# Optimization experiments

Measured on AMD Instinct MI355X. Metric: run time of the kernel, lower is better.

Reference implementation:

```python
import jax, jax.numpy as jnp
import numpy as np

EMBED_DIM = 2048
NUM_HEADS = 32
HEAD_DIM = EMBED_DIM // NUM_HEADS  # 64; only used as softmax scale
BATCH = 2
SEQ_LEN = 2048


def setup_inputs() -> dict:
    key = jax.random.key(0)
    ks = jax.random.split(key, 5)
    scale = 1.0 / np.sqrt(EMBED_DIM)
    x = jax.random.normal(ks[0], (BATCH, SEQ_LEN, EMBED_DIM), dtype=jnp.float32)
    Wq = jax.random.normal(ks[1], (EMBED_DIM, EMBED_DIM), dtype=jnp.float32) * scale
    Wk = jax.random.normal(ks[2], (EMBED_DIM, EMBED_DIM), dtype=jnp.float32) * scale
    Wv = jax.random.normal(ks[3], (EMBED_DIM, EMBED_DIM), dtype=jnp.float32) * scale
    Wo = jax.random.normal(ks[4], (EMBED_DIM, EMBED_DIM), dtype=jnp.float32) * scale
    return {"x": x, "Wq": Wq, "Wk": Wk, "Wv": Wv, "Wo": Wo}


def reference(x, Wq, Wk, Wv, Wo):
    # x: [b, s, e]
    q = jnp.einsum('bse,ef->bsf', x, Wq)  # [b, s, e]
    k = jnp.einsum('bse,ef->bsf', x, Wk)
    v = jnp.einsum('bse,ef->bsf', x, Wv)
    # NOTE: original transposes (1,2) WITHOUT splitting heads, so "attention"
    # is over the embed dimension: q^T k -> [b, e, e]
    qT = jnp.swapaxes(q, 1, 2)  # [b, e, s]
    kT = jnp.swapaxes(k, 1, 2)  # [b, e, s]
    vT = jnp.swapaxes(v, 1, 2)  # [b, e, s]
    attn_scores = jnp.einsum('bes,bfs->bef', qT, kT) / np.sqrt(HEAD_DIM)  # [b,e,e]
    attn_weights = jax.nn.softmax(attn_scores, axis=-1)
    attn_output = jnp.einsum('bef,bfs->bes', attn_weights, vT)  # [b, e, s]
    attn_output = jnp.swapaxes(attn_output, 1, 2)  # [b, s, e]
    return jnp.einsum('bse,ef->bsf', attn_output, Wo)
```

## Files before the change

kernel.cpp:

```cpp
#include <hip/hip_runtime.h>
#include <cstddef>
#include <cstdint>

constexpr int E     = 2048;
constexpr int SEQ   = 2048;
constexpr int BATCH = 2;
constexpr int BS    = BATCH * SEQ;

constexpr int BM = 128, BN = 128, BK = 64;

typedef _Float16 f16;
typedef f16  f16x4 __attribute__((ext_vector_type(4)));
typedef f16  f16x8 __attribute__((ext_vector_type(8)));
typedef float f32x4 __attribute__((ext_vector_type(4)));

#define GLOAD16(g, l)                                                   \
    __builtin_amdgcn_global_load_lds(                                   \
        (const __attribute__((address_space(1))) void*)(g),             \
        (__attribute__((address_space(3))) void*)(l), 16, 0, 0)

template <int EPI, typename CT>
__global__ __launch_bounds__(256) void gemm_f16(
    const f16* __restrict__ A, const f16* __restrict__ B, CT* __restrict__ C,
    int K, int lda, int ldb, int ldc,
    long long sA, long long sB, long long sC, float alpha)
{
    alignas(16) __shared__ f16 At[BM * BK];
    alignas(16) __shared__ f16 Bt[BN * BK];

    const int tid = threadIdx.x;
    const int l   = tid & 63;
    const int w   = tid >> 6;

    const int nwg  = gridDim.x * gridDim.y;
    const int flat = blockIdx.y * gridDim.x + blockIdx.x;
    const int cpx  = nwg >> 3;
    const int swz  = (flat & 7) * cpx + (flat >> 3);
    const int bx = swz % gridDim.x, by = swz / gridDim.x;
    const int m0 = by * BM, n0 = bx * BN;

    const f16* Ab = A + (size_t)blockIdx.z * sA;
    const f16* Bb = B + (size_t)blockIdx.z * sB;

    const int lr = l & 15;
    const int hi = l >> 4;
    const int wm = (w >> 1) * 64;
    const int wn = (w & 1) * 64;

    f32x4 acc[4][4] = {};

    for (int k0 = 0; k0 < K; k0 += BK) {
#pragma unroll
        for (int p = 0; p < 4; ++p) {
            const int ci  = p * 256 + tid;
            const int row = ci >> 3;
            const int sc  = (ci & 7) ^ (row & 7);
            GLOAD16(Ab + (size_t)(m0 + row) * lda + k0 + sc * 8,
                    At + p * 2048 + w * 512);
            GLOAD16(Bb + (size_t)(n0 + row) * ldb + k0 + sc * 8,
                    Bt + p * 2048 + w * 512);
        }
        __syncthreads();

        f16x8 af[4][2], bf[4][2];
#pragma unroll
        for (int i = 0; i < 4; ++i)
#pragma unroll
            for (int ks = 0; ks < 2; ++ks) {
                const int ar = wm + i * 16 + lr;
                const int ap = (ks * 4 + hi) ^ (ar & 7);
                af[i][ks] = *reinterpret_cast<const f16x8*>(At + ar * 64 + ap * 8);
                const int br = wn + i * 16 + lr;
                const int bp = (ks * 4 + hi) ^ (br & 7);
                bf[i][ks] = *reinterpret_cast<const f16x8*>(Bt + br * 64 + bp * 8);
            }
#pragma unroll
        for (int ks = 0; ks < 2; ++ks)
#pragma unroll
            for (int i = 0; i < 4; ++i)
#pragma unroll
                for (int j = 0; j < 4; ++j)
                    acc[i][j] = __builtin_amdgcn_mfma_f32_16x16x32_f16(
                        af[i][ks], bf[j][ks], acc[i][j], 0, 0, 0);
        __syncthreads();
    }

    if (EPI == 0) {
        CT* Cb = C + (size_t)blockIdx.z * sC;
#pragma unroll
        for (int i = 0; i < 4; ++i)
#pragma unroll
            for (int r = 0; r < 4; ++r) {
                const int row = m0 + wm + i * 16 + hi * 4 + r;
#pragma unroll
                for (int j = 0; j < 4; ++j) {
                    const int col = n0 + wn + j * 16 + lr;
                    Cb[(size_t)row * ldc + col] = (CT)(alpha * acc[i][j][r]);
                }
            }
    } else {
        f16* Cb = (f16*)C;
#pragma unroll
        for (int i = 0; i < 4; ++i) {
            const int rowb = m0 + wm + i * 16 + hi * 4;
            const long long base = ((long long)(rowb >> 11) << 22) + (rowb & 2047);
#pragma unroll
            for (int j = 0; j < 4; ++j) {
                const int col = n0 + wn + j * 16 + lr;
                f16x4 v = {(f16)(alpha * acc[i][j][0]), (f16)(alpha * acc[i][j][1]),
                           (f16)(alpha * acc[i][j][2]), (f16)(alpha * acc[i][j][3])};
                *reinterpret_cast<f16x4*>(Cb + base + (long long)col * 2048) = v;
            }
        }
    }
}

__global__ __launch_bounds__(256) void conv_x_f16(
    const float* __restrict__ x, f16* __restrict__ xc, int n4)
{
    int i = blockIdx.x * 256 + threadIdx.x;
    const int stride = gridDim.x * 256;
    for (; i < n4; i += stride) {
        const float4 v = reinterpret_cast<const float4*>(x)[i];
        f16x4 h = {(f16)v.x, (f16)v.y, (f16)v.z, (f16)v.w};
        reinterpret_cast<f16x4*>(xc)[i] = h;
    }
}

__global__ __launch_bounds__(256) void conv_wT(
    const float* __restrict__ W0, const float* __restrict__ W1,
    const float* __restrict__ W2, const float* __restrict__ W3,
    f16* __restrict__ O0, f16* __restrict__ O1,
    f16* __restrict__ O2, f16* __restrict__ O3)
{
    const float* src; f16* dst;
    switch (blockIdx.z) {
        case 0: src = W0; dst = O0; break;
        case 1: src = W1; dst = O1; break;
        case 2: src = W2; dst = O2; break;
        default: src = W3; dst = O3; break;
    }
    __shared__ f16 t[64][68];
    const int e0 = blockIdx.y * 64, f0 = blockIdx.x * 64;
    const int tid = threadIdx.x;
    const int tf = (tid & 15) * 4;
    const int te = tid >> 4;
#pragma unroll
    for (int p = 0; p < 4; ++p) {
        const int e = te + p * 16;
        const float4 v = *reinterpret_cast<const float4*>(
            &src[(size_t)(e0 + e) * 2048 + f0 + tf]);
        t[tf + 0][e] = (f16)v.x; t[tf + 1][e] = (f16)v.y;
        t[tf + 2][e] = (f16)v.z; t[tf + 3][e] = (f16)v.w;
    }
    __syncthreads();
#pragma unroll
    for (int p = 0; p < 4; ++p) {
        const int f = (tid >> 4) + p * 16;
        const int e = (tid & 15) * 4;
        const f16x4 v = *reinterpret_cast<const f16x4*>(&t[f][e]);
        *reinterpret_cast<f16x4*>(&dst[(size_t)(f0 + f) * 2048 + e0 + e]) = v;
    }
}

__global__ __launch_bounds__(256) void softmax_rows_f16(
    const float* __restrict__ S, f16* __restrict__ A)
{
    const float* row = S + (size_t)blockIdx.x * 2048;
    f16* arow = A + (size_t)blockIdx.x * 2048;
    const int tid = threadIdx.x;

    float4 v0 = reinterpret_cast<const float4*>(row)[tid];
    float4 v1 = reinterpret_cast<const float4*>(row)[tid + 256];

    float m = fmaxf(fmaxf(fmaxf(v0.x, v0.y), fmaxf(v0.z, v0.w)),
                    fmaxf(fmaxf(v1.x, v1.y), fmaxf(v1.z, v1.w)));
#pragma unroll
    for (int off = 32; off > 0; off >>= 1) m = fmaxf(m, __shfl_xor(m, off));

    __shared__ float red[8];
    if ((tid & 63) == 0) red[tid >> 6] = m;
    __syncthreads();
    m = fmaxf(fmaxf(red[0], red[1]), fmaxf(red[2], red[3]));

    v0.x = __expf(v0.x - m); v0.y = __expf(v0.y - m);
    v0.z = __expf(v0.z - m); v0.w = __expf(v0.w - m);
    v1.x = __expf(v1.x - m); v1.y = __expf(v1.y - m);
    v1.z = __expf(v1.z - m); v1.w = __expf(v1.w - m);

    float s = v0.x + v0.y + v0.z + v0.w + v1.x + v1.y + v1.z + v1.w;
#pragma unroll
    for (int off = 32; off > 0; off >>= 1) s += __shfl_xor(s, off);
    if ((tid & 63) == 0) red[4 + (tid >> 6)] = s;
    __syncthreads();
    s = red[4] + red[5] + red[6] + red[7];

    const float inv = 1.0f / s;
    f16x4 a0 = {(f16)(v0.x * inv), (f16)(v0.y * inv), (f16)(v0.z * inv), (f16)(v0.w * inv)};
    f16x4 a1 = {(f16)(v1.x * inv), (f16)(v1.y * inv), (f16)(v1.z * inv), (f16)(v1.w * inv)};
    reinterpret_cast<f16x4*>(arow)[tid]       = a0;
    reinterpret_cast<f16x4*>(arow)[tid + 256] = a1;
}

extern "C" void kernel_launch(void* const* d_in, const int* in_sizes, int n_in,
                              void* d_out, int out_size, void* d_ws, size_t ws_size,
                              hipStream_t stream)
{
    const float* x  = (const float*)d_in[0];
    const float* Wq = (const float*)d_in[1];
    const float* Wk = (const float*)d_in[2];
    const float* Wv = (const float*)d_in[3];
    const float* Wo = (const float*)d_in[4];
    float* out = (float*)d_out;

    f16* ws16 = (f16*)d_ws;
    const size_t MATE = (size_t)BS * E;
    const size_t WMAT = (size_t)E * E;
    f16* xc  = ws16;
    f16* WqT = xc  + MATE;
    f16* WkT = WqT + WMAT;
    f16* WvT = WkT + WMAT;
    f16* WoT = WvT + WMAT;
    f16* QT  = WoT + WMAT;
    f16* KT  = QT  + MATE;
    f16* V   = KT  + MATE;
    float* S = (float*)(V + MATE);
    f16* A   = QT;
    f16* AO  = KT;

    const dim3 blk(256);
    const long long BMATL = (long long)E * E;

    hipLaunchKernelGGL(conv_x_f16, dim3(2048), blk, 0, stream, x, xc, (int)(MATE / 4));
    hipLaunchKernelGGL(conv_wT, dim3(32, 32, 4), blk, 0, stream,
                       Wq, Wk, Wv, Wo, WqT, WkT, WvT, WoT);

    const dim3 gBig(E / BN, BS / BM, 1);
    const dim3 gSq (E / BN, E  / BM, BATCH);

    hipLaunchKernelGGL((gemm_f16<1, f16>), gBig, blk, 0, stream,
                       xc, WqT, QT, E, E, E, E, 0LL, 0LL, 0LL, 1.0f);
    hipLaunchKernelGGL((gemm_f16<1, f16>), gBig, blk, 0, stream,
                       xc, WkT, KT, E, E, E, E, 0LL, 0LL, 0LL, 1.0f);
    hipLaunchKernelGGL((gemm_f16<0, f16>), gBig, blk, 0, stream,
                       xc, WvT, V, E, E, E, E, 0LL, 0LL, 0LL, 1.0f);

    hipLaunchKernelGGL((gemm_f16<0, float>), gSq, blk, 0, stream,
                       QT, KT, S, SEQ, E, E, E, BMATL, BMATL, BMATL, 0.125f);

    hipLaunchKernelGGL(softmax_rows_f16, dim3(BATCH * E), blk, 0, stream, S, A);

    hipLaunchKernelGGL((gemm_f16<0, f16>), gSq, blk, 0, stream,
                       V, A, AO, E, E, E, E, BMATL, BMATL, BMATL, 1.0f);

    hipLaunchKernelGGL((gemm_f16<0, float>), gBig, blk, 0, stream,
                       AO, WoT, out, E, E, E, E, 0LL, 0LL, 0LL, 1.0f);
}
```

Before: 412.3 us.

## Double-buffer GEMM LDS tiles and fuse Q/K/V projections into one launch

The GEMM main loop now uses two LDS buffers and issues global-to-LDS loads for the next K tile before computing the current one, with one barrier per iteration. The aim is to hide global load latency behind the MFMA work. The three separate Q, K and V projection launches are merged into one kernel whose z-dimension selects the weight and the epilogue, which cuts launch gaps and tail effects. LDS per block doubles to 64 KB, which may reduce occupancy. The prefetch also relies on the single end-of-iteration barrier to keep the async LDS writes ordered, so a wait on those loads may be missing before the buffer is read.

After: 389.6 us. -5.5%, faster.

```diff
diff --git a/kernel.cpp b/kernel.cpp
--- a/kernel.cpp
+++ b/kernel.cpp
@@ -18,6 +18,78 @@
     __builtin_amdgcn_global_load_lds(                                   \
         (const __attribute__((address_space(1))) void*)(g),             \
         (__attribute__((address_space(3))) void*)(l), 16, 0, 0)
+
+__device__ __forceinline__ void gemm_core(
+    const f16* __restrict__ Ab, const f16* __restrict__ Bb,
+    int K, int lda, int ldb, int m0, int n0,
+    f16* At, f16* Bt, f32x4 acc[4][4])
+{
+    const int tid = threadIdx.x;
+    const int l  = tid & 63;
+    const int w  = tid >> 6;
+    const int lr = l & 15;
+    const int hi = l >> 4;
+    const int wm = (w >> 1) * 64;
+    const int wn = (w & 1) * 64;
+
+    auto stage = [&](int buf, int k0) {
+#pragma unroll
+        for (int p = 0; p < 4; ++p) {
+            const int ci  = p * 256 + tid;
+            const int row = ci >> 3;
+            const int sc  = (ci & 7) ^ (row & 7);
+            GLOAD16(Ab + (size_t)(m0 + row) * lda + k0 + sc * 8,
+                    At + buf * (BM * BK) + p * 2048 + w * 512);
+            GLOAD16(Bb + (size_t)(n0 + row) * ldb + k0 + sc * 8,
+                    Bt + buf * (BN * BK) + p * 2048 + w * 512);
+        }
+    };
+
+    stage(0, 0);
+    __syncthreads();
+
+    const int NT = K / BK;
+    int cur = 0;
+    for (int t = 0; t < NT; ++t) {
+        if (t + 1 < NT) stage(cur ^ 1, (t + 1) * BK);
+
+        const f16* Ac = At + cur * (BM * BK);
+        const f16* Bc = Bt + cur * (BN * BK);
+        f16x8 af[4][2], bf[4][2];
+#pragma unroll
+        for (int i = 0; i < 4; ++i)
+#pragma unroll
+            for (int ks = 0; ks < 2; ++ks) {
+                const int ar = wm + i * 16 + lr;
+                const int ap = (ks * 4 + hi) ^ (ar & 7);
+                af[i][ks] = *reinterpret_cast<const f16x8*>(Ac + ar * 64 + ap * 8);
+                const int br = wn + i * 16 + lr;
+                const int bp = (ks * 4 + hi) ^ (br & 7);
+                bf[i][ks] = *reinterpret_cast<const f16x8*>(Bc + br * 64 + bp * 8);
+            }
+#pragma unroll
+        for (int ks = 0; ks < 2; ++ks)
+#pragma unroll
+            for (int i = 0; i < 4; ++i)
+#pragma unroll
+                for (int j = 0; j < 4; ++j)
+                    acc[i][j] = __builtin_amdgcn_mfma_f32_16x16x32_f16(
+                        af[i][ks], bf[j][ks], acc[i][j], 0, 0, 0);
+
+        __syncthreads();
+        cur ^= 1;
+    }
+}
+
+__device__ __forceinline__ void swz_block(int gx, int gy, int& bx, int& by)
+{
+    const int nwg  = gx * gy;
+    const int flat = blockIdx.y * gx + blockIdx.x;
+    const int cpx  = nwg >> 3;
+    const int swz  = (flat & 7) * cpx + (flat >> 3);
+    bx = swz % gx;
+    by = swz / gx;
+}
 
 template <int EPI, typename CT>
 __global__ __launch_bounds__(256) void gemm_f16(
@@ -25,65 +97,20 @@
     int K, int lda, int ldb, int ldc,
     long long sA, long long sB, long long sC, float alpha)
 {
-    alignas(16) __shared__ f16 At[BM * BK];
-    alignas(16) __shared__ f16 Bt[BN * BK];
-
-    const int tid = threadIdx.x;
-    const int l   = tid & 63;
-    const int w   = tid >> 6;
-
-    const int nwg  = gridDim.x * gridDim.y;
-    const int flat = blockIdx.y * gridDim.x + blockIdx.x;
-    const int cpx  = nwg >> 3;
-    const int swz  = (flat & 7) * cpx + (flat >> 3);
-    const int bx = swz % gridDim.x, by = swz / gridDim.x;
+    alignas(16) __shared__ f16 At[2 * BM * BK];
+    alignas(16) __shared__ f16 Bt[2 * BN * BK];
+
+    int bx, by; swz_block(gridDim.x, gridDim.y, bx, by);
     const int m0 = by * BM, n0 = bx * BN;
 
-    const f16* Ab = A + (size_t)blockIdx.z * sA;
-    const f16* Bb = B + (size_t)blockIdx.z * sB;
-
-    const int lr = l & 15;
-    const int hi = l >> 4;
-    const int wm = (w >> 1) * 64;
-    const int wn = (w & 1) * 64;
-
     f32x4 acc[4][4] = {};
-
-    for (int k0 = 0; k0 < K; k0 += BK) {
-#pragma unroll
-        for (int p = 0; p < 4; ++p) {
-            const int ci  = p * 256 + tid;
-            const int row = ci >> 3;
-            const int sc  = (ci & 7) ^ (row & 7);
-            GLOAD16(Ab + (size_t)(m0 + row) * lda + k0 + sc * 8,
-                    At + p * 2048 + w * 512);
-            GLOAD16(Bb + (size_t)(n0 + row) * ldb + k0 + sc * 8,
-                    Bt + p * 2048 + w * 512);
-        }
-        __syncthreads();
-
-        f16x8 af[4][2], bf[4][2];
-#pragma unroll
-        for (int i = 0; i < 4; ++i)
-#pragma unroll
-            for (int ks = 0; ks < 2; ++ks) {
-                const int ar = wm + i * 16 + lr;
-                const int ap = (ks * 4 + hi) ^ (ar & 7);
-                af[i][ks] = *reinterpret_cast<const f16x8*>(At + ar * 64 + ap * 8);
-                const int br = wn + i * 16 + lr;
-                const int bp = (ks * 4 + hi) ^ (br & 7);
-                bf[i][ks] = *reinterpret_cast<const f16x8*>(Bt + br * 64 + bp * 8);
-            }
-#pragma unroll
-        for (int ks = 0; ks < 2; ++ks)
-#pragma unroll
-            for (int i = 0; i < 4; ++i)
-#pragma unroll
-                for (int j = 0; j < 4; ++j)
-                    acc[i][j] = __builtin_amdgcn_mfma_f32_16x16x32_f16(
-                        af[i][ks], bf[j][ks], acc[i][j], 0, 0, 0);
-        __syncthreads();
-    }
+    gemm_core(A + (size_t)blockIdx.z * sA, B + (size_t)blockIdx.z * sB,
+              K, lda, ldb, m0, n0, At, Bt, acc);
+
+    const int l  = threadIdx.x & 63;
+    const int w  = threadIdx.x >> 6;
+    const int lr = l & 15, hi = l >> 4;
+    const int wm = (w >> 1) * 64, wn = (w & 1) * 64;
 
     if (EPI == 0) {
         CT* Cb = C + (size_t)blockIdx.z * sC;
@@ -109,6 +136,58 @@
                 const int col = n0 + wn + j * 16 + lr;
                 f16x4 v = {(f16)(alpha * acc[i][j][0]), (f16)(alpha * acc[i][j][1]),
                            (f16)(alpha * acc[i][j][2]), (f16)(alpha * acc[i][j][3])};
+                *reinterpret_cast<f16x4*>(Cb + base + (long long)col * 2048) = v;
+            }
+        }
+    }
+}
+
+__global__ __launch_bounds__(256) void qkv_f16(
+    const f16* __restrict__ xc,
+    const f16* __restrict__ WqT, const f16* __restrict__ WkT,
+    const f16* __restrict__ WvT,
+    f16* __restrict__ QT, f16* __restrict__ KT, f16* __restrict__ V)
+{
+    alignas(16) __shared__ f16 At[2 * BM * BK];
+    alignas(16) __shared__ f16 Bt[2 * BN * BK];
+
+    const int z = blockIdx.z;
+    const f16* B = (z == 0) ? WqT : (z == 1) ? WkT : WvT;
+
+    int bx, by; swz_block(gridDim.x, gridDim.y, bx, by);
+    const int m0 = by * BM, n0 = bx * BN;
+
+    f32x4 acc[4][4] = {};
+    gemm_core(xc, B, E, E, E, m0, n0, At, Bt, acc);
+
+    const int l  = threadIdx.x & 63;
+    const int w  = threadIdx.x >> 6;
+    const int lr = l & 15, hi = l >> 4;
+    const int wm = (w >> 1) * 64, wn = (w & 1) * 64;
+
+    if (z == 2) {
+#pragma unroll
+        for (int i = 0; i < 4; ++i)
+#pragma unroll
+            for (int r = 0; r < 4; ++r) {
+                const int row = m0 + wm + i * 16 + hi * 4 + r;
+#pragma unroll
+                for (int j = 0; j < 4; ++j) {
+                    const int col = n0 + wn + j * 16 + lr;
+                    V[(size_t)row * E + col] = (f16)acc[i][j][r];
+                }
+            }
+    } else {
+        f16* Cb = (z == 0) ? QT : KT;
+#pragma unroll
+        for (int i = 0; i < 4; ++i) {
+            const int rowb = m0 + wm + i * 16 + hi * 4;
+            const long long base = ((long long)(rowb >> 11) << 22) + (rowb & 2047);
+#pragma unroll
+            for (int j = 0; j < 4; ++j) {
+                const int col = n0 + wn + j * 16 + lr;
+                f16x4 v = {(f16)acc[i][j][0], (f16)acc[i][j][1],
+                           (f16)acc[i][j][2], (f16)acc[i][j][3]};
                 *reinterpret_cast<f16x4*>(Cb + base + (long long)col * 2048) = v;
             }
         }
@@ -238,12 +317,8 @@
     const dim3 gBig(E / BN, BS / BM, 1);
     const dim3 gSq (E / BN, E  / BM, BATCH);
 
-    hipLaunchKernelGGL((gemm_f16<1, f16>), gBig, blk, 0, stream,
-                       xc, WqT, QT, E, E, E, E, 0LL, 0LL, 0LL, 1.0f);
-    hipLaunchKernelGGL((gemm_f16<1, f16>), gBig, blk, 0, stream,
-                       xc, WkT, KT, E, E, E, E, 0LL, 0LL, 0LL, 1.0f);
-    hipLaunchKernelGGL((gemm_f16<0, f16>), gBig, blk, 0, stream,
-                       xc, WvT, V, E, E, E, E, 0LL, 0LL, 0LL, 1.0f);
+    hipLaunchKernelGGL(qkv_f16, dim3(E / BN, BS / BM, 3), blk, 0, stream,
+                       xc, WqT, WkT, WvT, QT, KT, V);
 
     hipLaunchKernelGGL((gemm_f16<0, float>), gSq, blk, 0, stream,
                        QT, KT, S, SEQ, E, E, E, BMATL, BMATL, BMATL, 0.125f);
```
